# Kernel optimization log

Measured on AMD Instinct MI355X. Metric: run time of the kernel, lower is better.

Reference implementation:

```python
import jax, jax.numpy as jnp
import numpy as np


def _conv1x1(x, w, b):
    # x: [B, Cin, H, W]; w: [Cout, Cin, 1, 1]; b: [Cout]
    y = jnp.einsum('bchw,oc->bohw', x, w[:, :, 0, 0])
    return y + b[None, :, None, None]


def setup_inputs() -> dict:
    key = jax.random.key(0)
    ks = jax.random.split(key, 9)
    B, C, H, W = 8, 256, 64, 64
    Cq = C // 4
    sc = 0.05
    return {
        'x': jax.random.normal(ks[0], (B, C, H, W), jnp.float32),
        'query_weight': jax.random.normal(ks[1], (Cq, C, 1, 1), jnp.float32) * sc,
        'query_bias': jax.random.normal(ks[2], (Cq,), jnp.float32) * sc,
        'key_weight': jax.random.normal(ks[3], (Cq, C, 1, 1), jnp.float32) * sc,
        'key_bias': jax.random.normal(ks[4], (Cq,), jnp.float32) * sc,
        'value_weight': jax.random.normal(ks[5], (C, C, 1, 1), jnp.float32) * sc,
        'value_bias': jax.random.normal(ks[6], (C,), jnp.float32) * sc,
        'gamma_weight': jax.random.normal(ks[7], (C, C, 1, 1), jnp.float32) * sc,
        'gamma_bias': jax.random.normal(ks[8], (C,), jnp.float32) * sc,
    }


def reference(x, query_weight, query_bias, key_weight, key_bias,
              value_weight, value_bias, gamma_weight, gamma_bias):
    B, C, H, W = x.shape
    N = H * W
    q = _conv1x1(x, query_weight, query_bias).reshape(B, -1, N)   # [B, Cq, N]
    k = _conv1x1(x, key_weight, key_bias).reshape(B, -1, N)       # [B, Cq, N]
    v = _conv1x1(x, value_weight, value_bias).reshape(B, C, N)    # [B, C, N]
    # energy[b, i, j] = sum_c q[b, c, i] * k[b, c, j]
    energy = jnp.einsum('bci,bcj->bij', q, k)                     # [B, N, N]
    energy = jax.nn.elu(energy) / N
    out = jnp.einsum('bcn,bnm->bcm', v, energy).reshape(B, C, H, W)
    return _conv1x1(out, gamma_weight, gamma_bias)
```

## Files before the change

### kernel.cpp

```cpp
#include <hip/hip_runtime.h>
#include <cmath>

#define BB 8
#define CC 256
#define CQ 64
#define NN 4096
constexpr float INV_N = 1.0f / 4096.0f;

typedef __attribute__((ext_vector_type(8))) short short8;
typedef __attribute__((ext_vector_type(4))) short short4v;
typedef __attribute__((ext_vector_type(4))) float float4v;

__device__ __forceinline__ short f2bf(float f) {
  union { float f; unsigned u; } x; x.f = f;
  unsigned r = x.u + 0x7fffu + ((x.u >> 16) & 1u);
  return (short)(r >> 16);
}

__global__ __launch_bounds__(256, 2) void qkv_kernel(
    const float* __restrict__ X,
    const float* __restrict__ wq, const float* __restrict__ bq,
    const float* __restrict__ wk, const float* __restrict__ bk,
    const float* __restrict__ wv, const float* __restrict__ bv,
    short* __restrict__ qt, short* __restrict__ kt, short* __restrict__ vbf) {
  __shared__ short xt[64 * 272];
  __shared__ short Os[64 * 72];
  const int tid = threadIdx.x;
  const int wid = tid >> 6;
  const int lane = tid & 63, quad = lane >> 4, l16 = lane & 15;
  const int n0 = blockIdx.x * 64, b = blockIdx.y;

#pragma unroll 4
  for (int p = 0; p < 16; ++p) {
    const int idx = p * 256 + tid;
    const int c = idx >> 4;
    const int n4 = (idx & 15) * 4;
    const float4 x4 = *reinterpret_cast<const float4*>(
        &X[((size_t)b * CC + c) * NN + n0 + n4]);
    xt[(n4 + 0) * 272 + c] = f2bf(x4.x);
    xt[(n4 + 1) * 272 + c] = f2bf(x4.y);
    xt[(n4 + 2) * 272 + c] = f2bf(x4.z);
    xt[(n4 + 3) * 272 + c] = f2bf(x4.w);
  }
  __syncthreads();

  for (int ch = 0; ch < 6; ++ch) {
    const float* W; const float* bias; int obase;
    if (ch == 0)      { W = wq; bias = bq; obase = 0; }
    else if (ch == 1) { W = wk; bias = bk; obase = 0; }
    else { W = wv + (size_t)(ch - 2) * 64 * CC; bias = bv + (ch - 2) * 64; obase = (ch - 2) * 64; }

    float4v acc[4];
#pragma unroll
    for (int tm = 0; tm < 4; ++tm) acc[tm] = float4v{0.f, 0.f, 0.f, 0.f};

#pragma unroll
    for (int kk = 0; kk < 8; ++kk) {
      const float* wp = &W[(size_t)(wid * 16 + l16) * CC + kk * 32 + quad * 8];
      const float4v w0 = *reinterpret_cast<const float4v*>(wp);
      const float4v w1 = *reinterpret_cast<const float4v*>(wp + 4);
      short8 a;
      a[0] = f2bf(w0[0]); a[1] = f2bf(w0[1]); a[2] = f2bf(w0[2]); a[3] = f2bf(w0[3]);
      a[4] = f2bf(w1[0]); a[5] = f2bf(w1[1]); a[6] = f2bf(w1[2]); a[7] = f2bf(w1[3]);
#pragma unroll
      for (int tm = 0; tm < 4; ++tm) {
        const short8 bfrag = *reinterpret_cast<const short8*>(
            &xt[(tm * 16 + l16) * 272 + kk * 32 + quad * 8]);
        acc[tm] = __builtin_amdgcn_mfma_f32_16x16x32_bf16(a, bfrag, acc[tm], 0, 0, 0);
      }
    }

    if (ch < 2) {
      short* dst = (ch == 0) ? qt : kt;
#pragma unroll
      for (int tm = 0; tm < 4; ++tm) {
        short4v pk;
#pragma unroll
        for (int r = 0; r < 4; ++r)
          pk[r] = f2bf(acc[tm][r] + bias[wid * 16 + quad * 4 + r]);
        *reinterpret_cast<short4v*>(
            &dst[((size_t)b * NN + n0 + tm * 16 + l16) * 64 + wid * 16 + quad * 4]) = pk;
      }
    } else {
      __syncthreads();
#pragma unroll
      for (int tm = 0; tm < 4; ++tm)
#pragma unroll
        for (int r = 0; r < 4; ++r)
          Os[(wid * 16 + quad * 4 + r) * 72 + tm * 16 + l16] =
              f2bf(acc[tm][r] + bias[wid * 16 + quad * 4 + r]);
      __syncthreads();
      const int o = tid >> 2, ng = (tid & 3) * 16;
      const short8 s0 = *reinterpret_cast<const short8*>(&Os[o * 72 + ng]);
      const short8 s1 = *reinterpret_cast<const short8*>(&Os[o * 72 + ng + 8]);
      short* vp = &vbf[((size_t)b * CC + obase + o) * NN + n0 + ng];
      *reinterpret_cast<short8*>(vp) = s0;
      *reinterpret_cast<short8*>(vp + 8) = s1;
    }
  }
}

__global__ __launch_bounds__(256, 2) void attn_kernel(
    const short* __restrict__ qt, const short* __restrict__ kt,
    const short* __restrict__ vbf, const float* __restrict__ Wg,
    const float* __restrict__ bg, float* __restrict__ out) {
  __shared__ short smem[16896];
  short* Es0 = smem;
  short* Es1 = smem + 4608;
  short* Outs = smem;

  const int tid = threadIdx.x;
  const int wid = tid >> 6;
  const int lane = tid & 63, quad = lane >> 4, l16 = lane & 15;
  const int m0 = blockIdx.x * 64, b = blockIdx.y;

  short8 bkf[4][2];
#pragma unroll
  for (int tm = 0; tm < 4; ++tm)
#pragma unroll
    for (int kk = 0; kk < 2; ++kk)
      bkf[tm][kk] = *reinterpret_cast<const short8*>(
          &kt[((size_t)b * NN + m0 + tm * 16 + l16) * 64 + kk * 32 + quad * 8]);

  const short* qrow = &qt[((size_t)b * NN + wid * 16 + l16) * 64 + quad * 8];
  const short* vrow[4];
#pragma unroll
  for (int tc = 0; tc < 4; ++tc)
    vrow[tc] = &vbf[((size_t)b * CC + wid * 64 + tc * 16 + l16) * NN + quad * 8];

  float4v acc[4][4];
#pragma unroll
  for (int i = 0; i < 4; ++i)
#pragma unroll
    for (int j = 0; j < 4; ++j) acc[i][j] = float4v{0.f, 0.f, 0.f, 0.f};

  short8 aq0 = *reinterpret_cast<const short8*>(qrow);
  short8 aq1 = *reinterpret_cast<const short8*>(qrow + 32);

  for (int it = 0; it < 64; ++it) {
    const int nb = it * 64;
    short* Esw = (it & 1) ? Es1 : Es0;

    short8 av[4][2];
#pragma unroll
    for (int tc = 0; tc < 4; ++tc) {
      av[tc][0] = *reinterpret_cast<const short8*>(vrow[tc] + nb);
      av[tc][1] = *reinterpret_cast<const short8*>(vrow[tc] + nb + 32);
    }

    float4v s[4];
#pragma unroll
    for (int tm = 0; tm < 4; ++tm) {
      float4v t = {0.f, 0.f, 0.f, 0.f};
      t = __builtin_amdgcn_mfma_f32_16x16x32_bf16(aq0, bkf[tm][0], t, 0, 0, 0);
      t = __builtin_amdgcn_mfma_f32_16x16x32_bf16(aq1, bkf[tm][1], t, 0, 0, 0);
      s[tm] = t;
    }

    const short8 aq0n = *reinterpret_cast<const short8*>(qrow + (size_t)(it + 1) * 64 * 64);
    const short8 aq1n = *reinterpret_cast<const short8*>(qrow + (size_t)(it + 1) * 64 * 64 + 32);

#pragma unroll
    for (int tm = 0; tm < 4; ++tm) {
      short4v pk;
#pragma unroll
      for (int r = 0; r < 4; ++r) {
        float sv = s[tm][r];
        sv = (sv > 0.f) ? sv : (__expf(sv) - 1.f);
        pk[r] = f2bf(sv * INV_N);
      }
      *reinterpret_cast<short4v*>(
          &Esw[(tm * 16 + l16) * 72 + wid * 16 + quad * 4]) = pk;
    }
    __syncthreads();

#pragma unroll
    for (int tm = 0; tm < 4; ++tm) {
      const short8 be0 = *reinterpret_cast<const short8*>(
          &Esw[(tm * 16 + l16) * 72 + quad * 8]);
      const short8 be1 = *reinterpret_cast<const short8*>(
          &Esw[(tm * 16 + l16) * 72 + 32 + quad * 8]);
#pragma unroll
      for (int tc = 0; tc < 4; ++tc) {
        acc[tc][tm] = __builtin_amdgcn_mfma_f32_16x16x32_bf16(av[tc][0], be0, acc[tc][tm], 0, 0, 0);
        acc[tc][tm] = __builtin_amdgcn_mfma_f32_16x16x32_bf16(av[tc][1], be1, acc[tc][tm], 0, 0, 0);
      }
    }
    aq0 = aq0n; aq1 = aq1n;
  }

  __syncthreads();
#pragma unroll
  for (int tc = 0; tc < 4; ++tc)
#pragma unroll
    for (int tm = 0; tm < 4; ++tm) {
      short4v pk;
#pragma unroll
      for (int r = 0; r < 4; ++r) pk[r] = f2bf(acc[tc][tm][r]);
      *reinterpret_cast<short4v*>(
          &Outs[(tm * 16 + l16) * 264 + wid * 64 + tc * 16 + quad * 4]) = pk;
    }
  __syncthreads();

#pragma unroll
  for (int i = 0; i < 4; ++i)
#pragma unroll
    for (int j = 0; j < 4; ++j) acc[i][j] = float4v{0.f, 0.f, 0.f, 0.f};

  for (int ks8 = 0; ks8 < 8; ++ks8) {
    short8 ag[4];
#pragma unroll
    for (int to = 0; to < 4; ++to) {
      const float* wp =
          &Wg[(size_t)(wid * 64 + to * 16 + l16) * CC + ks8 * 32 + quad * 8];
      const float4v w0 = *reinterpret_cast<const float4v*>(wp);
      const float4v w1 = *reinterpret_cast<const float4v*>(wp + 4);
      short8 a;
      a[0] = f2bf(w0[0]); a[1] = f2bf(w0[1]); a[2] = f2bf(w0[2]); a[3] = f2bf(w0[3]);
      a[4] = f2bf(w1[0]); a[5] = f2bf(w1[1]); a[6] = f2bf(w1[2]); a[7] = f2bf(w1[3]);
      ag[to] = a;
    }
    short8 bo[4];
#pragma unroll
    for (int tm = 0; tm < 4; ++tm)
      bo[tm] = *reinterpret_cast<const short8*>(
          &Outs[(tm * 16 + l16) * 264 + ks8 * 32 + quad * 8]);
#pragma unroll
    for (int to = 0; to < 4; ++to)
#pragma unroll
      for (int tm = 0; tm < 4; ++tm)
        acc[to][tm] =
            __builtin_amdgcn_mfma_f32_16x16x32_bf16(ag[to], bo[tm], acc[to][tm], 0, 0, 0);
  }

#pragma unroll
  for (int to = 0; to < 4; ++to) {
#pragma unroll
    for (int r = 0; r < 4; ++r) {
      const int o = wid * 64 + to * 16 + quad * 4 + r;
      const float bgv = bg[o];
#pragma unroll
      for (int tm = 0; tm < 4; ++tm) {
        out[((size_t)b * CC + o) * NN + m0 + tm * 16 + l16] =
            acc[to][tm][r] + bgv;
      }
    }
  }
}

extern "C" void kernel_launch(void* const* d_in, const int* in_sizes, int n_in,
                              void* d_out, int out_size, void* d_ws,
                              size_t ws_size, hipStream_t stream) {
  const float* x  = (const float*)d_in[0];
  const float* wq = (const float*)d_in[1];
  const float* bq = (const float*)d_in[2];
  const float* wk = (const float*)d_in[3];
  const float* bk = (const float*)d_in[4];
  const float* wv = (const float*)d_in[5];
  const float* bv = (const float*)d_in[6];
  const float* wg = (const float*)d_in[7];
  const float* bg = (const float*)d_in[8];
  float* out = (float*)d_out;

  short* qt  = (short*)d_ws;
  short* kt  = qt + (size_t)BB * NN * CQ;
  short* vbf = kt + (size_t)BB * NN * CQ;

  qkv_kernel<<<dim3(NN / 64, BB), 256, 0, stream>>>(x, wq, bq, wk, bk, wv, bv,
                                                    qt, kt, vbf);
  attn_kernel<<<dim3(NN / 64, BB), 256, 0, stream>>>(qt, kt, vbf, wg, bg, out);
}
```

Before: 283.7 us.

## Fold output projection into value weights and halve attention tile width

Precomputes Wg·Wv and Wg·bv in a prep kernel so the attention kernel no longer runs the final 1x1 conv GEMM, and preconverts Q/K weights to bf16. Both qkv and attn kernels now use 32-column tiles with higher occupancy bounds, and the x staging buffer in LDS is XOR-swizzled. Removing the gamma epilogue cuts per-block work and LDS, but smaller tiles double V streaming per output and add a launch. Folding the weights also changes bf16 rounding order.

```diff
diff --git a/kernel.cpp b/kernel.cpp
--- a/kernel.cpp
+++ b/kernel.cpp
@@ -17,106 +17,165 @@
   return (short)(r >> 16);
 }
 
-__global__ __launch_bounds__(256, 2) void qkv_kernel(
+__global__ __launch_bounds__(256) void prep_kernel(
+    const float* __restrict__ wq, const float* __restrict__ wk,
+    const float* __restrict__ wv, const float* __restrict__ wg,
+    const float* __restrict__ bv,
+    short* __restrict__ wqbf, short* __restrict__ wkbf,
+    short* __restrict__ wvpbf, float* __restrict__ bvp) {
+  const int bx = blockIdx.x;
+  const int tid = threadIdx.x;
+  if (bx < 64) {
+    const int o0 = (bx >> 3) * 32, c0 = (bx & 7) * 32;
+    const int cc = tid & 31, oo = tid >> 5;
+    float acc[4] = {0.f, 0.f, 0.f, 0.f};
+    for (int u = 0; u < 256; ++u) {
+      const float xv = wv[(size_t)u * 256 + c0 + cc];
+#pragma unroll
+      for (int i = 0; i < 4; ++i)
+        acc[i] += wg[(size_t)(o0 + oo * 4 + i) * 256 + u] * xv;
+    }
+#pragma unroll
+    for (int i = 0; i < 4; ++i)
+      wvpbf[(size_t)(o0 + oo * 4 + i) * 256 + c0 + cc] = f2bf(acc[i]);
+  } else if (bx == 64) {
+#pragma unroll 4
+    for (int t = 0; t < 16; ++t) {
+      const int idx = (t * 256 + tid) * 4;
+      const float4 a = *reinterpret_cast<const float4*>(&wq[idx]);
+      short4v p; p.x = f2bf(a.x); p.y = f2bf(a.y); p.z = f2bf(a.z); p.w = f2bf(a.w);
+      *reinterpret_cast<short4v*>(&wqbf[idx]) = p;
+      const float4 b4 = *reinterpret_cast<const float4*>(&wk[idx]);
+      short4v q4; q4.x = f2bf(b4.x); q4.y = f2bf(b4.y); q4.z = f2bf(b4.z); q4.w = f2bf(b4.w);
+      *reinterpret_cast<short4v*>(&wkbf[idx]) = q4;
+    }
+  } else {
+    float acc = 0.f;
+    for (int u = 0; u < 256; ++u) acc += wg[(size_t)tid * 256 + u] * bv[u];
+    bvp[tid] = acc;
+  }
+}
+
+__global__ __launch_bounds__(256, 4) void qkv_kernel(
     const float* __restrict__ X,
-    const float* __restrict__ wq, const float* __restrict__ bq,
-    const float* __restrict__ wk, const float* __restrict__ bk,
-    const float* __restrict__ wv, const float* __restrict__ bv,
-    short* __restrict__ qt, short* __restrict__ kt, short* __restrict__ vbf) {
-  __shared__ short xt[64 * 272];
-  __shared__ short Os[64 * 72];
+    const short* __restrict__ wqbf, const short* __restrict__ wkbf,
+    const short* __restrict__ wvpbf,
+    const float* __restrict__ bq, const float* __restrict__ bk,
+    const float* __restrict__ bvp,
+    short* __restrict__ qt, short* __restrict__ kt, short* __restrict__ vt) {
+  __shared__ short smem[8448 + 2560];
+  short* xt = smem;
+  short* Os = smem + 8448;
+
   const int tid = threadIdx.x;
   const int wid = tid >> 6;
   const int lane = tid & 63, quad = lane >> 4, l16 = lane & 15;
-  const int n0 = blockIdx.x * 64, b = blockIdx.y;
-
-#pragma unroll 4
-  for (int p = 0; p < 16; ++p) {
+  const int b = blockIdx.x, n0 = blockIdx.y * 32;
+
+#pragma unroll
+  for (int p = 0; p < 8; ++p) {
     const int idx = p * 256 + tid;
-    const int c = idx >> 4;
-    const int n4 = (idx & 15) * 4;
+    const int c = idx >> 3;
+    const int n4 = (idx & 7) * 4;
     const float4 x4 = *reinterpret_cast<const float4*>(
         &X[((size_t)b * CC + c) * NN + n0 + n4]);
-    xt[(n4 + 0) * 272 + c] = f2bf(x4.x);
-    xt[(n4 + 1) * 272 + c] = f2bf(x4.y);
-    xt[(n4 + 2) * 272 + c] = f2bf(x4.z);
-    xt[(n4 + 3) * 272 + c] = f2bf(x4.w);
+    const int sw = (n4 >> 2) & 7;
+    const int chp = (c >> 3) ^ sw;
+    const int cols = chp * 8 + (c & 7);
+    xt[(n4 + 0) * 264 + cols] = f2bf(x4.x);
+    xt[(n4 + 1) * 264 + cols] = f2bf(x4.y);
+    xt[(n4 + 2) * 264 + cols] = f2bf(x4.z);
+    xt[(n4 + 3) * 264 + cols] = f2bf(x4.w);
   }
   __syncthreads();
 
+  const short* Wsrc[6] = {wqbf, wkbf, wvpbf, wvpbf + 64 * 256,
+                          wvpbf + 128 * 256, wvpbf + 192 * 256};
+  const int arow = wid * 16 + l16;
+
+  short8 curA[8];
+#pragma unroll
+  for (int kk = 0; kk < 8; ++kk)
+    curA[kk] = *reinterpret_cast<const short8*>(
+        &Wsrc[0][(size_t)arow * 256 + kk * 32 + quad * 8]);
+
+#pragma unroll
   for (int ch = 0; ch < 6; ++ch) {
-    const float* W; const float* bias; int obase;
-    if (ch == 0)      { W = wq; bias = bq; obase = 0; }
-    else if (ch == 1) { W = wk; bias = bk; obase = 0; }
-    else { W = wv + (size_t)(ch - 2) * 64 * CC; bias = bv + (ch - 2) * 64; obase = (ch - 2) * 64; }
-
-    float4v acc[4];
-#pragma unroll
-    for (int tm = 0; tm < 4; ++tm) acc[tm] = float4v{0.f, 0.f, 0.f, 0.f};
-
+    short8 nxtA[8];
+    if (ch < 5) {
+#pragma unroll
+      for (int kk = 0; kk < 8; ++kk)
+        nxtA[kk] = *reinterpret_cast<const short8*>(
+            &Wsrc[ch + 1][(size_t)arow * 256 + kk * 32 + quad * 8]);
+    }
+
+    float4v acc2[2];
+    acc2[0] = float4v{0.f, 0.f, 0.f, 0.f};
+    acc2[1] = float4v{0.f, 0.f, 0.f, 0.f};
 #pragma unroll
     for (int kk = 0; kk < 8; ++kk) {
-      const float* wp = &W[(size_t)(wid * 16 + l16) * CC + kk * 32 + quad * 8];
-      const float4v w0 = *reinterpret_cast<const float4v*>(wp);
-      const float4v w1 = *reinterpret_cast<const float4v*>(wp + 4);
-      short8 a;
-      a[0] = f2bf(w0[0]); a[1] = f2bf(w0[1]); a[2] = f2bf(w0[2]); a[3] = f2bf(w0[3]);
-      a[4] = f2bf(w1[0]); a[5] = f2bf(w1[1]); a[6] = f2bf(w1[2]); a[7] = f2bf(w1[3]);
-#pragma unroll
-      for (int tm = 0; tm < 4; ++tm) {
+#pragma unroll
+      for (int tm = 0; tm < 2; ++tm) {
+        const int row = tm * 16 + l16;
+        const int swr = (row >> 2) & 7;
         const short8 bfrag = *reinterpret_cast<const short8*>(
-            &xt[(tm * 16 + l16) * 272 + kk * 32 + quad * 8]);
-        acc[tm] = __builtin_amdgcn_mfma_f32_16x16x32_bf16(a, bfrag, acc[tm], 0, 0, 0);
+            &xt[row * 264 + ((kk * 4 + quad) ^ swr) * 8]);
+        acc2[tm] = __builtin_amdgcn_mfma_f32_16x16x32_bf16(curA[kk], bfrag,
+                                                           acc2[tm], 0, 0, 0);
       }
     }
 
     if (ch < 2) {
+      const float* bias = (ch == 0) ? bq : bk;
+      const float4v bv4 = *reinterpret_cast<const float4v*>(
+          &bias[wid * 16 + quad * 4]);
       short* dst = (ch == 0) ? qt : kt;
 #pragma unroll
-      for (int tm = 0; tm < 4; ++tm) {
+      for (int tm = 0; tm < 2; ++tm) {
         short4v pk;
 #pragma unroll
+        for (int r = 0; r < 4; ++r) pk[r] = f2bf(acc2[tm][r] + bv4[r]);
+        *reinterpret_cast<short4v*>(
+            &dst[((size_t)b * NN + n0 + tm * 16 + l16) * 64 + wid * 16 +
+                 quad * 4]) = pk;
+      }
+    } else {
+      const float4v bv4 = *reinterpret_cast<const float4v*>(
+          &bvp[(ch - 2) * 64 + wid * 16 + quad * 4]);
+      __syncthreads();
+#pragma unroll
+      for (int tm = 0; tm < 2; ++tm)
+#pragma unroll
         for (int r = 0; r < 4; ++r)
-          pk[r] = f2bf(acc[tm][r] + bias[wid * 16 + quad * 4 + r]);
-        *reinterpret_cast<short4v*>(
-            &dst[((size_t)b * NN + n0 + tm * 16 + l16) * 64 + wid * 16 + quad * 4]) = pk;
-      }
-    } else {
+          Os[(wid * 16 + quad * 4 + r) * 40 + tm * 16 + l16] =
+              f2bf(acc2[tm][r] + bv4[r]);
       __syncthreads();
-#pragma unroll
-      for (int tm = 0; tm < 4; ++tm)
-#pragma unroll
-        for (int r = 0; r < 4; ++r)
-          Os[(wid * 16 + quad * 4 + r) * 72 + tm * 16 + l16] =
-              f2bf(acc[tm][r] + bias[wid * 16 + quad * 4 + r]);
-      __syncthreads();
-      const int o = tid >> 2, ng = (tid & 3) * 16;
-      const short8 s0 = *reinterpret_cast<const short8*>(&Os[o * 72 + ng]);
-      const short8 s1 = *reinterpret_cast<const short8*>(&Os[o * 72 + ng + 8]);
-      short* vp = &vbf[((size_t)b * CC + obase + o) * NN + n0 + ng];
-      *reinterpret_cast<short8*>(vp) = s0;
-      *reinterpret_cast<short8*>(vp + 8) = s1;
-    }
-  }
-}
-
-__global__ __launch_bounds__(256, 2) void attn_kernel(
+      const int o = tid >> 2, ng = (tid & 3) * 8;
+      const short8 s0 = *reinterpret_cast<const short8*>(&Os[o * 40 + ng]);
+      *reinterpret_cast<short8*>(
+          &vt[((size_t)b * CC + (ch - 2) * 64 + o) * NN + n0 + ng]) = s0;
+    }
+#pragma unroll
+    for (int kk = 0; kk < 8; ++kk) curA[kk] = nxtA[kk];
+  }
+}
+
+__global__ __launch_bounds__(256, 4) void attn_kernel(
     const short* __restrict__ qt, const short* __restrict__ kt,
-    const short* __restrict__ vbf, const float* __restrict__ Wg,
-    const float* __restrict__ bg, float* __restrict__ out) {
-  __shared__ short smem[16896];
+    const short* __restrict__ vt, const float* __restrict__ bg,
+    float* __restrict__ out) {
+  __shared__ short smem[4608];
   short* Es0 = smem;
-  short* Es1 = smem + 4608;
-  short* Outs = smem;
+  short* Es1 = smem + 2304;
 
   const int tid = threadIdx.x;
   const int wid = tid >> 6;
   const int lane = tid & 63, quad = lane >> 4, l16 = lane & 15;
-  const int m0 = blockIdx.x * 64, b = blockIdx.y;
-
-  short8 bkf[4][2];
-#pragma unroll
-  for (int tm = 0; tm < 4; ++tm)
+  const int b = blockIdx.x, m0 = blockIdx.y * 32;
+
+  short8 bkf[2][2];
+#pragma unroll
+  for (int tm = 0; tm < 2; ++tm)
 #pragma unroll
     for (int kk = 0; kk < 2; ++kk)
       bkf[tm][kk] = *reinterpret_cast<const short8*>(
@@ -126,13 +185,13 @@
   const short* vrow[4];
 #pragma unroll
   for (int tc = 0; tc < 4; ++tc)
-    vrow[tc] = &vbf[((size_t)b * CC + wid * 64 + tc * 16 + l16) * NN + quad * 8];
-
-  float4v acc[4][4];
+    vrow[tc] = &vt[((size_t)b * CC + wid * 64 + tc * 16 + l16) * NN + quad * 8];
+
+  float4v acc[4][2];
 #pragma unroll
   for (int i = 0; i < 4; ++i)
 #pragma unroll
-    for (int j = 0; j < 4; ++j) acc[i][j] = float4v{0.f, 0.f, 0.f, 0.f};
+    for (int j = 0; j < 2; ++j) acc[i][j] = float4v{0.f, 0.f, 0.f, 0.f};
 
   short8 aq0 = *reinterpret_cast<const short8*>(qrow);
   short8 aq1 = *reinterpret_cast<const short8*>(qrow + 32);
@@ -148,101 +207,62 @@
       av[tc][1] = *reinterpret_cast<const short8*>(vrow[tc] + nb + 32);
     }
 
-    float4v s[4];
-#pragma unroll
-    for (int tm = 0; tm < 4; ++tm) {
+    float4v s[2];
+#pragma unroll
+    for (int tm2 = 0; tm2 < 2; ++tm2) {
       float4v t = {0.f, 0.f, 0.f, 0.f};
-      t = __builtin_amdgcn_mfma_f32_16x16x32_bf16(aq0, bkf[tm][0], t, 0, 0, 0);
-      t = __builtin_amdgcn_mfma_f32_16x16x32_bf16(aq1, bkf[tm][1], t, 0, 0, 0);
-      s[tm] = t;
-    }
-
-    const short8 aq0n = *reinterpret_cast<const short8*>(qrow + (size_t)(it + 1) * 64 * 64);
-    const short8 aq1n = *reinterpret_cast<const short8*>(qrow + (size_t)(it + 1) * 64 * 64 + 32);
-
-#pragma unroll
-    for (int tm = 0; tm < 4; ++tm) {
+      t = __builtin_amdgcn_mfma_f32_16x16x32_bf16(aq0, bkf[tm2][0], t, 0, 0, 0);
+      t = __builtin_amdgcn_mfma_f32_16x16x32_bf16(aq1, bkf[tm2][1], t, 0, 0, 0);
+      s[tm2] = t;
+    }
+
+    const short8 aq0n =
+        *reinterpret_cast<const short8*>(qrow + (size_t)(it + 1) * 64 * 64);
+    const short8 aq1n =
+        *reinterpret_cast<const short8*>(qrow + (size_t)(it + 1) * 64 * 64 + 32);
+
+#pragma unroll
+    for (int tm2 = 0; tm2 < 2; ++tm2) {
       short4v pk;
 #pragma unroll
       for (int r = 0; r < 4; ++r) {
-        float sv = s[tm][r];
+        float sv = s[tm2][r];
         sv = (sv > 0.f) ? sv : (__expf(sv) - 1.f);
         pk[r] = f2bf(sv * INV_N);
       }
       *reinterpret_cast<short4v*>(
-          &Esw[(tm * 16 + l16) * 72 + wid * 16 + quad * 4]) = pk;
+          &Esw[(tm2 * 16 + l16) * 72 + wid * 16 + quad * 4]) = pk;
     }
     __syncthreads();
 
 #pragma unroll
-    for (int tm = 0; tm < 4; ++tm) {
+    for (int tm = 0; tm < 2; ++tm) {
       const short8 be0 = *reinterpret_cast<const short8*>(
           &Esw[(tm * 16 + l16) * 72 + quad * 8]);
       const short8 be1 = *reinterpret_cast<const short8*>(
           &Esw[(tm * 16 + l16) * 72 + 32 + quad * 8]);
 #pragma unroll
       for (int tc = 0; tc < 4; ++tc) {
-        acc[tc][tm] = __builtin_amdgcn_mfma_f32_16x16x32_bf16(av[tc][0], be0, acc[tc][tm], 0, 0, 0);
-        acc[tc][tm] = __builtin_amdgcn_mfma_f32_16x16x32_bf16(av[tc][1], be1, acc[tc][tm], 0, 0, 0);
+        acc[tc][tm] = __builtin_amdgcn_mfma_f32_16x16x32_bf16(
+            av[tc][0], be0, acc[tc][tm], 0, 0, 0);
+        acc[tc][tm] = __builtin_amdgcn_mfma_f32_16x16x32_bf16(
+            av[tc][1], be1, acc[tc][tm], 0, 0, 0);
       }
     }
     aq0 = aq0n; aq1 = aq1n;
   }
 
-  __syncthreads();
-#pragma unroll
-  for (int tc = 0; tc < 4; ++tc)
-#pragma unroll
-    for (int tm = 0; tm < 4; ++tm) {
-      short4v pk;
-#pragma unroll
-      for (int r = 0; r < 4; ++r) pk[r] = f2bf(acc[tc][tm][r]);
-      *reinterpret_cast<short4v*>(
-          &Outs[(tm * 16 + l16) * 264 + wid * 64 + tc * 16 + quad * 4]) = pk;
-    }
-  __syncthreads();
-
-#pragma unroll
-  for (int i = 0; i < 4; ++i)
-#pragma unroll
-    for (int j = 0; j < 4; ++j) acc[i][j] = float4v{0.f, 0.f, 0.f, 0.f};
-
-  for (int ks8 = 0; ks8 < 8; ++ks8) {
-    short8 ag[4];
-#pragma unroll
-    for (int to = 0; to < 4; ++to) {
-      const float* wp =
-          &Wg[(size_t)(wid * 64 + to * 16 + l16) * CC + ks8 * 32 + quad * 8];
-      const float4v w0 = *reinterpret_cast<const float4v*>(wp);
-      const float4v w1 = *reinterpret_cast<const float4v*>(wp + 4);
-      short8 a;
-      a[0] = f2bf(w0[0]); a[1] = f2bf(w0[1]); a[2] = f2bf(w0[2]); a[3] = f2bf(w0[3]);
-      a[4] = f2bf(w1[0]); a[5] = f2bf(w1[1]); a[6] = f2bf(w1[2]); a[7] = f2bf(w1[3]);
-      ag[to] = a;
-    }
-    short8 bo[4];
-#pragma unroll
-    for (int tm = 0; tm < 4; ++tm)
-      bo[tm] = *reinterpret_cast<const short8*>(
-          &Outs[(tm * 16 + l16) * 264 + ks8 * 32 + quad * 8]);
-#pragma unroll
-    for (int to = 0; to < 4; ++to)
-#pragma unroll
-      for (int tm = 0; tm < 4; ++tm)
-        acc[to][tm] =
-            __builtin_amdgcn_mfma_f32_16x16x32_bf16(ag[to], bo[tm], acc[to][tm], 0, 0, 0);
-  }
-
-#pragma unroll
-  for (int to = 0; to < 4; ++to) {
+#pragma unroll
+  for (int tc = 0; tc < 4; ++tc) {
+    const float4v bg4 = *reinterpret_cast<const float4v*>(
+        &bg[wid * 64 + tc * 16 + quad * 4]);
 #pragma unroll
     for (int r = 0; r < 4; ++r) {
-      const int o = wid * 64 + to * 16 + quad * 4 + r;
-      const float bgv = bg[o];
-#pragma unroll
-      for (int tm = 0; tm < 4; ++tm) {
-        out[((size_t)b * CC + o) * NN + m0 + tm * 16 + l16] =
-            acc[to][tm][r] + bgv;
+      const int c = wid * 64 + tc * 16 + quad * 4 + r;
+#pragma unroll
+      for (int tm = 0; tm < 2; ++tm) {
+        out[((size_t)b * CC + c) * NN + m0 + tm * 16 + l16] =
+            acc[tc][tm][r] + bg4[r];
       }
     }
   }
@@ -262,11 +282,17 @@
   const float* bg = (const float*)d_in[8];
   float* out = (float*)d_out;
 
-  short* qt  = (short*)d_ws;
-  short* kt  = qt + (size_t)BB * NN * CQ;
-  short* vbf = kt + (size_t)BB * NN * CQ;
-
-  qkv_kernel<<<dim3(NN / 64, BB), 256, 0, stream>>>(x, wq, bq, wk, bk, wv, bv,
-                                                    qt, kt, vbf);
-  attn_kernel<<<dim3(NN / 64, BB), 256, 0, stream>>>(qt, kt, vbf, wg, bg, out);
-}
+  short* qt    = (short*)d_ws;
+  short* kt    = qt + (size_t)BB * NN * CQ;
+  short* vt    = kt + (size_t)BB * NN * CQ;
+  short* wqbf  = vt + (size_t)BB * CC * NN;
+  short* wkbf  = wqbf + (size_t)CQ * CC;
+  short* wvpbf = wkbf + (size_t)CQ * CC;
+  float* bvp   = (float*)(wvpbf + (size_t)CC * CC);
+
+  prep_kernel<<<dim3(66), 256, 0, stream>>>(wq, wk, wv, wg, bv,
+                                            wqbf, wkbf, wvpbf, bvp);
+  qkv_kernel<<<dim3(BB, NN / 32), 256, 0, stream>>>(
+      x, wqbf, wkbf, wvpbf, bq, bk, bvp, qt, kt, vt);
+  attn_kernel<<<dim3(BB, NN / 32), 256, 0, stream>>>(qt, kt, vt, bg, out);
+}
```

Result: slower. 423.5 us (+49.3%).
